# Kernel tuning notes

Hardware: AMD Instinct MI355X
Metric: run time of the kernel (lower is better)

## Reference

```python
import jax, jax.numpy as jnp
import numpy as np

VOCAB = 128
HIDDEN = 256


def setup_inputs() -> dict:
    key = jax.random.key(0)
    ks = jax.random.split(key, 8)
    B, S = 64, 2048
    # first feature channel: event-type ids stored as floats (module does .long())
    ev = jax.random.randint(ks[0], (B, S, 1), 0, VOCAB).astype(jnp.float32)
    num = jax.random.normal(ks[1], (B, S, 7), dtype=jnp.float32)
    X = jnp.concatenate([ev, num], axis=-1)  # [B,S,8]
    emb_table = jax.random.normal(ks[2], (VOCAB, 124), dtype=jnp.float32) * 0.1
    W_num = jax.random.normal(ks[3], (4, 7), dtype=jnp.float32) * 0.3
    b_num = jnp.zeros((4,), dtype=jnp.float32)
    W_conv = jax.random.normal(ks[4], (3 * HIDDEN, 128), dtype=jnp.float32) * 0.08
    b_conv = jnp.zeros((3 * HIDDEN,), dtype=jnp.float32)
    W_out = jax.random.normal(ks[5], (1, HIDDEN), dtype=jnp.float32) * 0.06
    b_out = jnp.zeros((1,), dtype=jnp.float32)
    return {"X": X, "emb_table": emb_table, "W_num": W_num, "b_num": b_num,
            "W_conv": W_conv, "b_conv": b_conv, "W_out": W_out, "b_out": b_out}


def reference(X, emb_table, W_num, b_num, W_conv, b_conv, W_out, b_out):
    # X: [B,S,8] -- channel 0 = event id, channels 1: = numeric attrs
    event = jax.lax.stop_gradient(X[:, :, 0]).astype(jnp.int32)   # [B,S]
    numeric = X[:, :, 1:]                                          # [B,S,7]
    emb = emb_table[event]                                         # [B,S,124]
    tn = numeric @ W_num.T + b_num                                 # [B,S,4]
    comb = jnp.concatenate([emb, tn], axis=-1)                     # [B,S,128]
    # Conv1d with kernel_size=1 == pointwise linear to 3*hidden gates
    gates = comb @ W_conv.T + b_conv                               # [B,S,3H]
    gates = jnp.transpose(gates, (1, 0, 2))                        # [S,B,3H]
    Z, F, O = jnp.split(gates, 3, axis=2)
    Z = jnp.tanh(Z)
    F = jax.nn.sigmoid(F)
    O = jax.nn.sigmoid(O)

    def step(h, zfo):
        z, f, o = zfo
        h = f * h + (1.0 - f) * z
        return h, o * h

    h0 = jnp.zeros(Z.shape[1:], dtype=Z.dtype)                     # [B,H]
    _, hs = jax.lax.scan(step, h0, (Z, F, O))                      # hs: [S,B,H]
    final_rep = hs[-1]                                             # [B,H]
    # dropout is identity at inference (dropout=0 / eval)
    return final_rep @ W_out.T + b_out                             # [B,1]
```

## Files before the change

### kernel.cpp

```cpp
#include <hip/hip_runtime.h>


typedef float    f32x2 __attribute__((ext_vector_type(2)));
typedef float    f32x4 __attribute__((ext_vector_type(4)));
typedef _Float16 f16x2 __attribute__((ext_vector_type(2)));

#define NB 64
#define NS 2048
#define NH 256
#define CHUNKS 32
#define STEPS (NS / CHUNKS)
#define LOG2E 1.4426950408889634f
#define PAD 129
#define JH 128

__global__ __launch_bounds__(256) void precompute_kernel(
    const float* __restrict__ X,
    const float* __restrict__ emb,
    const float* __restrict__ Wn,
    const float* __restrict__ bn,
    const float* __restrict__ Wc,
    const float* __restrict__ bc,
    f16x2* __restrict__ G2h,
    float* __restrict__ Go,
    f32x2* __restrict__ Wg4,
    float* __restrict__ Wgo4,
    f32x4* __restrict__ XpA,
    float* __restrict__ XpB)
{
    const int tid = threadIdx.x;
    const int blk = blockIdx.x;

    if (blk < 256) {
        __shared__ float M[124 * PAD];
        __shared__ float P[3][2][128];
        {
            const int e = tid >> 1, half = tid & 1;
            const f32x4* er4 = (const f32x4*)(emb + (size_t)e * 124);
            #pragma unroll
            for (int i = 0; i < 16; ++i) {
                const int idx = half * 16 + i;
                if (idx < 31) {
                    const f32x4 v = er4[idx];
                    const int k0 = idx * 4;
                    M[(k0 + 0) * PAD + e] = v.x;
                    M[(k0 + 1) * PAD + e] = v.y;
                    M[(k0 + 2) * PAD + e] = v.z;
                    M[(k0 + 3) * PAD + e] = v.w;
                }
            }
        }
        __syncthreads();

        const int e = tid & 127;
        const int h = tid >> 7;
        const int j = blk;
        const int k0 = h * 62;

        const float* __restrict__ wzr = Wc + (size_t)j * 128;
        const float* __restrict__ wfr = Wc + (size_t)(j + 256) * 128;
        const float* __restrict__ wor = Wc + (size_t)(j + 512) * 128;

        float az = 0.f, af = 0.f, ao = 0.f;
        #pragma unroll 31
        for (int i = 0; i < 62; ++i) {
            const int k = k0 + i;
            const float mv = M[k * PAD + e];
            az = fmaf(wzr[k], mv, az);
            af = fmaf(wfr[k], mv, af);
            ao = fmaf(wor[k], mv, ao);
        }
        P[0][h][e] = az; P[1][h][e] = af; P[2][h][e] = ao;
        __syncthreads();

        if (h == 0) {
            float sz = P[0][0][e] + P[0][1][e] + bc[j];
            float sf = P[1][0][e] + P[1][1][e] + bc[j + 256];
            float so = P[2][0][e] + P[2][1][e] + bc[j + 512];
            #pragma unroll
            for (int m = 0; m < 4; ++m) {
                const float bm = bn[m];
                sz = fmaf(wzr[124 + m], bm, sz);
                sf = fmaf(wfr[124 + m], bm, sf);
                so = fmaf(wor[124 + m], bm, so);
            }
            G2h[(size_t)e * NH + j] = (f16x2){(_Float16)(sz * (-2.0f * LOG2E)),
                                              (_Float16)(sf * (-LOG2E))};
            Go[(size_t)e * NH + j] = so * (-LOG2E);
        }
    } else if (blk == 256) {
        const int j = tid;
        #pragma unroll
        for (int m = 0; m < 4; ++m) {
            const float wz = Wc[(size_t)j * 128 + 124 + m];
            const float wf = Wc[(size_t)(j + 256) * 128 + 124 + m];
            const float wo = Wc[(size_t)(j + 512) * 128 + 124 + m];
            Wg4[m * NH + j]  = (f32x2){wz * (-2.0f * LOG2E), wf * (-LOG2E)};
            Wgo4[m * NH + j] = wo * (-LOG2E);
        }
    } else {
        const f32x4* X4 = (const f32x4*)X;
        float wn[4][7];
        #pragma unroll
        for (int m = 0; m < 4; ++m)
            #pragma unroll
            for (int n = 0; n < 7; ++n) wn[m][n] = Wn[m * 7 + n];

        const int base = (blk - 257) * 1024 + tid;
        #pragma unroll
        for (int u = 0; u < 4; ++u) {
            const int idx = base + u * 256;
            const f32x4 xa = X4[(size_t)idx * 2];
            const f32x4 xb = X4[(size_t)idx * 2 + 1];
            const int eo = ((int)xa.x) << 9;
            const float xs[7] = {xa.y, xa.z, xa.w, xb.x, xb.y, xb.z, xb.w};
            float y[4];
            #pragma unroll
            for (int m = 0; m < 4; ++m) {
                float s = 0.0f;
                #pragma unroll
                for (int n = 0; n < 7; ++n) s = fmaf(wn[m][n], xs[n], s);
                y[m] = s;
            }
            XpA[idx] = (f32x4){__int_as_float(eo), y[0], y[1], y[2]};
            XpB[idx] = y[3];
        }
    }
}

__global__ __launch_bounds__(1024) void scan_kernel(
    const f32x4* __restrict__ XpA,
    const float* __restrict__ XpB,
    const f16x2* __restrict__ G2h,
    const float* __restrict__ Go,
    const f32x2* __restrict__ Wg4,
    const float* __restrict__ Wgo4,
    float* __restrict__ AB,
    float* __restrict__ Olast)
{
    __shared__ f16x2 T[128 * JH];

    const int tid = threadIdx.x;
    const int jbase = blockIdx.y * JH;

    {
        const uint4* __restrict__ src = (const uint4*)G2h;
        uint4* dst = (uint4*)T;
        const int colbase = jbase >> 2;
        #pragma unroll
        for (int i = tid; i < 4096; i += 1024) {
            const int e = i >> 5, c16 = i & 31;
            dst[i] = src[e * 64 + colbase + c16];
        }
    }
    __syncthreads();

    const int slice = tid >> 7;
    const int jj = tid & (JH - 1);
    const int widx = (int)blockIdx.x * 8 + slice;
    const int b = widx >> 5;
    const int c = widx & (CHUNKS - 1);
    const int j = jbase + jj;

    const f32x4* __restrict__ xa = XpA + ((size_t)b * NS + (size_t)c * STEPS);
    const float* __restrict__ xb = XpB + ((size_t)b * NS + (size_t)c * STEPS);
    const char*  __restrict__ Tb = (const char*)T;
    const int jj4 = jj * 4;

    const f32x2 w0 = Wg4[0 * NH + j];
    const f32x2 w1 = Wg4[1 * NH + j];
    const f32x2 w2 = Wg4[2 * NH + j];
    const f32x2 w3 = Wg4[3 * NH + j];

    float A = 1.0f, Bv = 0.0f;
    #pragma unroll
    for (int t = 0; t < STEPS; ++t) {
        const f32x4 ra = xa[t];
        const float y3 = xb[t];
        const unsigned eo = (unsigned)__float_as_int(ra.x);
        const f16x2 gh = *(const f16x2*)(Tb + eo + jj4);
        f32x2 g = (f32x2){(float)gh.x, (float)gh.y};
        g = __builtin_elementwise_fma(w0, (f32x2){ra.y, ra.y}, g);
        g = __builtin_elementwise_fma(w1, (f32x2){ra.z, ra.z}, g);
        g = __builtin_elementwise_fma(w2, (f32x2){ra.w, ra.w}, g);
        g = __builtin_elementwise_fma(w3, (f32x2){y3, y3}, g);

        const float ez = __builtin_amdgcn_exp2f(g.x);
        const float ef = __builtin_amdgcn_exp2f(g.y);
        const float az = 1.0f + ez, af = 1.0f + ef;
        const float r = __builtin_amdgcn_rcpf(az * af);
        const float f = r * az;
        const float z = fmaf(2.0f, r * af, -1.0f);

        A *= f;
        Bv = fmaf(f, Bv - z, z);
    }

    AB[(((size_t)c * NB + b) * 2 + 0) * NH + j] = A;
    AB[(((size_t)c * NB + b) * 2 + 1) * NH + j] = Bv;

    if (c == CHUNKS - 1) {
        const f32x4 la = xa[STEPS - 1];
        const float ly3 = xb[STEPS - 1];
        const size_t eo = (size_t)(unsigned)__float_as_int(la.x);
        float go = *(const float*)((const char*)Go + (eo << 1) + (size_t)j * 4);
        go = fmaf(Wgo4[0 * NH + j], la.y, go);
        go = fmaf(Wgo4[1 * NH + j], la.z, go);
        go = fmaf(Wgo4[2 * NH + j], la.w, go);
        go = fmaf(Wgo4[3 * NH + j], ly3, go);
        Olast[b * NH + j] = __builtin_amdgcn_rcpf(1.0f + __builtin_amdgcn_exp2f(go));
    }
}

__global__ __launch_bounds__(256) void combine_kernel(
    const float* __restrict__ AB,
    const float* __restrict__ Olast,
    const float* __restrict__ Wout,
    const float* __restrict__ bout,
    float* __restrict__ out)
{
    const int b = blockIdx.x;
    const int j = threadIdx.x;

    float h = 0.0f;
    #pragma unroll 8
    for (int c = 0; c < CHUNKS; ++c) {
        const float A  = AB[(((size_t)c * NB + b) * 2 + 0) * NH + j];
        const float Bv = AB[(((size_t)c * NB + b) * 2 + 1) * NH + j];
        h = fmaf(A, h, Bv);
    }
    float v = Olast[b * NH + j] * h * Wout[j];

    #pragma unroll
    for (int off = 32; off > 0; off >>= 1) v += __shfl_down(v, off);
    __shared__ float red[4];
    if ((j & 63) == 0) red[j >> 6] = v;
    __syncthreads();
    if (j == 0) out[b] = red[0] + red[1] + red[2] + red[3] + bout[0];
}

extern "C" void kernel_launch(void* const* d_in, const int* in_sizes, int n_in,
                              void* d_out, int out_size, void* d_ws, size_t ws_size,
                              hipStream_t stream) {
    const float* X    = (const float*)d_in[0];
    const float* emb  = (const float*)d_in[1];
    const float* Wn   = (const float*)d_in[2];
    const float* bn   = (const float*)d_in[3];
    const float* Wc   = (const float*)d_in[4];
    const float* bc   = (const float*)d_in[5];
    const float* Wout = (const float*)d_in[6];
    const float* bout = (const float*)d_in[7];
    float* out = (float*)d_out;

    char* w = (char*)d_ws;
    f16x2* G2h  = (f16x2*)w;   w += 128 * NH * sizeof(f16x2);
    float* Go   = (float*)w;   w += 128 * NH * sizeof(float);
    f32x2* Wg4  = (f32x2*)w;   w += 4 * NH * sizeof(f32x2);
    float* Wgo4 = (float*)w;   w += 4 * NH * sizeof(float);
    float* AB   = (float*)w;   w += (size_t)CHUNKS * NB * 2 * NH * sizeof(float);
    float* Ol   = (float*)w;   w += NB * NH * sizeof(float);
    f32x4* XpA  = (f32x4*)w;   w += (size_t)NB * NS * sizeof(f32x4);
    float* XpB  = (float*)w;   w += (size_t)NB * NS * sizeof(float);

    precompute_kernel<<<385, 256, 0, stream>>>(X, emb, Wn, bn, Wc, bc,
                                               G2h, Go, Wg4, Wgo4, XpA, XpB);
    dim3 gridS(256, 2);
    scan_kernel<<<gridS, 1024, 0, stream>>>(XpA, XpB, G2h, Go, Wg4, Wgo4, AB, Ol);
    combine_kernel<<<NB, 256, 0, stream>>>(AB, Ol, Wout, bout, out);
}
```

Measured before the change: 40.39 us.

## Split scan into 64 chunks with two independent chains per thread

The scan is re-partitioned: the sequence is cut into twice as many chunks, each block covers a quarter of the hidden units, and each thread advances two independent chunk recurrences at once. The per-block LDS table slice shrinks to match the smaller hidden slice, and the event-offset encoding is adjusted to the new row stride. The aim is to shorten serial dependency chains and overlap latency through instruction-level parallelism and higher occupancy. In exchange, the combine step has more chunk partials to merge, and each thread holds more registers.

```diff
diff --git a/kernel.cpp b/kernel.cpp
--- a/kernel.cpp
+++ b/kernel.cpp
@@ -8,11 +8,11 @@
 #define NB 64
 #define NS 2048
 #define NH 256
-#define CHUNKS 32
+#define CHUNKS 64
 #define STEPS (NS / CHUNKS)
 #define LOG2E 1.4426950408889634f
 #define PAD 129
-#define JH 128
+#define JH 64
 
 __global__ __launch_bounds__(256) void precompute_kernel(
     const float* __restrict__ X,
@@ -112,7 +112,7 @@
             const int idx = base + u * 256;
             const f32x4 xa = X4[(size_t)idx * 2];
             const f32x4 xb = X4[(size_t)idx * 2 + 1];
-            const int eo = ((int)xa.x) << 9;
+            const int eo = ((int)xa.x) << 8;
             const float xs[7] = {xa.y, xa.z, xa.w, xb.x, xb.y, xb.z, xb.w};
             float y[4];
             #pragma unroll
@@ -128,7 +128,7 @@
     }
 }
 
-__global__ __launch_bounds__(1024) void scan_kernel(
+__global__ __launch_bounds__(512, 4) void scan_kernel(
     const f32x4* __restrict__ XpA,
     const float* __restrict__ XpB,
     const f16x2* __restrict__ G2h,
@@ -141,29 +141,34 @@
     __shared__ f16x2 T[128 * JH];
 
     const int tid = threadIdx.x;
-    const int jbase = blockIdx.y * JH;
+    const int jq = blockIdx.y;
+    const int jbase = jq * JH;
 
     {
         const uint4* __restrict__ src = (const uint4*)G2h;
         uint4* dst = (uint4*)T;
-        const int colbase = jbase >> 2;
-        #pragma unroll
-        for (int i = tid; i < 4096; i += 1024) {
-            const int e = i >> 5, c16 = i & 31;
+        const int colbase = jq * 16;
+        #pragma unroll
+        for (int i = tid; i < 2048; i += 512) {
+            const int e = i >> 4, c16 = i & 15;
             dst[i] = src[e * 64 + colbase + c16];
         }
     }
     __syncthreads();
 
-    const int slice = tid >> 7;
     const int jj = tid & (JH - 1);
-    const int widx = (int)blockIdx.x * 8 + slice;
-    const int b = widx >> 5;
-    const int c = widx & (CHUNKS - 1);
+    const int row = tid >> 6;
     const int j = jbase + jj;
-
-    const f32x4* __restrict__ xa = XpA + ((size_t)b * NS + (size_t)c * STEPS);
-    const float* __restrict__ xb = XpB + ((size_t)b * NS + (size_t)c * STEPS);
+    const int widx0 = (int)blockIdx.x * 16 + row;
+    const int widx1 = widx0 + 8;
+    const int b  = widx0 >> 6;
+    const int c0 = widx0 & (CHUNKS - 1);
+    const int c1 = widx1 & (CHUNKS - 1);
+
+    const f32x4* __restrict__ xa0 = XpA + ((size_t)b * NS + (size_t)c0 * STEPS);
+    const float* __restrict__ xb0 = XpB + ((size_t)b * NS + (size_t)c0 * STEPS);
+    const f32x4* __restrict__ xa1 = XpA + ((size_t)b * NS + (size_t)c1 * STEPS);
+    const float* __restrict__ xb1 = XpB + ((size_t)b * NS + (size_t)c1 * STEPS);
     const char*  __restrict__ Tb = (const char*)T;
     const int jj4 = jj * 4;
 
@@ -172,38 +177,57 @@
     const f32x2 w2 = Wg4[2 * NH + j];
     const f32x2 w3 = Wg4[3 * NH + j];
 
-    float A = 1.0f, Bv = 0.0f;
+    float A0 = 1.0f, B0 = 0.0f, A1 = 1.0f, B1 = 0.0f;
     #pragma unroll
     for (int t = 0; t < STEPS; ++t) {
-        const f32x4 ra = xa[t];
-        const float y3 = xb[t];
-        const unsigned eo = (unsigned)__float_as_int(ra.x);
-        const f16x2 gh = *(const f16x2*)(Tb + eo + jj4);
-        f32x2 g = (f32x2){(float)gh.x, (float)gh.y};
-        g = __builtin_elementwise_fma(w0, (f32x2){ra.y, ra.y}, g);
-        g = __builtin_elementwise_fma(w1, (f32x2){ra.z, ra.z}, g);
-        g = __builtin_elementwise_fma(w2, (f32x2){ra.w, ra.w}, g);
-        g = __builtin_elementwise_fma(w3, (f32x2){y3, y3}, g);
-
-        const float ez = __builtin_amdgcn_exp2f(g.x);
-        const float ef = __builtin_amdgcn_exp2f(g.y);
-        const float az = 1.0f + ez, af = 1.0f + ef;
-        const float r = __builtin_amdgcn_rcpf(az * af);
-        const float f = r * az;
-        const float z = fmaf(2.0f, r * af, -1.0f);
-
-        A *= f;
-        Bv = fmaf(f, Bv - z, z);
-    }
-
-    AB[(((size_t)c * NB + b) * 2 + 0) * NH + j] = A;
-    AB[(((size_t)c * NB + b) * 2 + 1) * NH + j] = Bv;
-
-    if (c == CHUNKS - 1) {
-        const f32x4 la = xa[STEPS - 1];
-        const float ly3 = xb[STEPS - 1];
+        const f32x4 ra0 = xa0[t];
+        const float ry0 = xb0[t];
+        const f32x4 ra1 = xa1[t];
+        const float ry1 = xb1[t];
+        const unsigned eo0 = (unsigned)__float_as_int(ra0.x);
+        const unsigned eo1 = (unsigned)__float_as_int(ra1.x);
+        const f16x2 gh0 = *(const f16x2*)(Tb + eo0 + jj4);
+        const f16x2 gh1 = *(const f16x2*)(Tb + eo1 + jj4);
+
+        f32x2 g0 = (f32x2){(float)gh0.x, (float)gh0.y};
+        g0 = __builtin_elementwise_fma(w0, (f32x2){ra0.y, ra0.y}, g0);
+        g0 = __builtin_elementwise_fma(w1, (f32x2){ra0.z, ra0.z}, g0);
+        g0 = __builtin_elementwise_fma(w2, (f32x2){ra0.w, ra0.w}, g0);
+        g0 = __builtin_elementwise_fma(w3, (f32x2){ry0, ry0}, g0);
+
+        f32x2 g1 = (f32x2){(float)gh1.x, (float)gh1.y};
+        g1 = __builtin_elementwise_fma(w0, (f32x2){ra1.y, ra1.y}, g1);
+        g1 = __builtin_elementwise_fma(w1, (f32x2){ra1.z, ra1.z}, g1);
+        g1 = __builtin_elementwise_fma(w2, (f32x2){ra1.w, ra1.w}, g1);
+        g1 = __builtin_elementwise_fma(w3, (f32x2){ry1, ry1}, g1);
+
+        const float ez0 = __builtin_amdgcn_exp2f(g0.x);
+        const float ef0 = __builtin_amdgcn_exp2f(g0.y);
+        const float ez1 = __builtin_amdgcn_exp2f(g1.x);
+        const float ef1 = __builtin_amdgcn_exp2f(g1.y);
+        const float az0 = 1.0f + ez0, af0 = 1.0f + ef0;
+        const float az1 = 1.0f + ez1, af1 = 1.0f + ef1;
+        const float r0 = __builtin_amdgcn_rcpf(az0 * af0);
+        const float r1 = __builtin_amdgcn_rcpf(az1 * af1);
+        const float f0 = r0 * az0;
+        const float f1 = r1 * az1;
+        const float z0 = fmaf(2.0f, r0 * af0, -1.0f);
+        const float z1 = fmaf(2.0f, r1 * af1, -1.0f);
+
+        A0 *= f0; B0 = fmaf(f0, B0 - z0, z0);
+        A1 *= f1; B1 = fmaf(f1, B1 - z1, z1);
+    }
+
+    AB[(((size_t)c0 * NB + b) * 2 + 0) * NH + j] = A0;
+    AB[(((size_t)c0 * NB + b) * 2 + 1) * NH + j] = B0;
+    AB[(((size_t)c1 * NB + b) * 2 + 0) * NH + j] = A1;
+    AB[(((size_t)c1 * NB + b) * 2 + 1) * NH + j] = B1;
+
+    if (c1 == CHUNKS - 1) {
+        const f32x4 la = xa1[STEPS - 1];
+        const float ly3 = xb1[STEPS - 1];
         const size_t eo = (size_t)(unsigned)__float_as_int(la.x);
-        float go = *(const float*)((const char*)Go + (eo << 1) + (size_t)j * 4);
+        float go = *(const float*)((const char*)Go + (eo << 2) + (size_t)j * 4);
         go = fmaf(Wgo4[0 * NH + j], la.y, go);
         go = fmaf(Wgo4[1 * NH + j], la.z, go);
         go = fmaf(Wgo4[2 * NH + j], la.w, go);
@@ -264,7 +288,7 @@
 
     precompute_kernel<<<385, 256, 0, stream>>>(X, emb, Wn, bn, Wc, bc,
                                                G2h, Go, Wg4, Wgo4, XpA, XpB);
-    dim3 gridS(256, 2);
-    scan_kernel<<<gridS, 1024, 0, stream>>>(XpA, XpB, G2h, Go, Wg4, Wgo4, AB, Ol);
+    dim3 gridS(256, 4);
+    scan_kernel<<<gridS, 512, 0, stream>>>(XpA, XpB, G2h, Go, Wg4, Wgo4, AB, Ol);
     combine_kernel<<<NB, 256, 0, stream>>>(AB, Ol, Wout, bout, out);
 }
```

Measured after the change: 45.29 us. 1.12x slower.

## Pack per-step inputs into one 16-byte record and software-pipeline scan loads

Applied to the files above, without the earlier changes.

The two per-step input streams (an f32x4 plus a separate float) are merged into a single 16-byte record by storing the last two numeric projections as packed fp16. The scan loop now prefetches records three steps ahead and the LDS gate lookup one step ahead, using register ring buffers with unroll 4. This aims to cut global load instructions and hide load latency in the sequential recurrence. The cost is reduced precision on two projected inputs, and reads that run past each chunk's end, which the padded buffer absorbs.

```diff
diff --git a/kernel.cpp b/kernel.cpp
--- a/kernel.cpp
+++ b/kernel.cpp
@@ -13,6 +13,8 @@
 #define LOG2E 1.4426950408889634f
 #define PAD 129
 #define JH 128
+
+union f16x2_f32 { f16x2 h; float f; };
 
 __global__ __launch_bounds__(256) void precompute_kernel(
     const float* __restrict__ X,
@@ -25,8 +27,7 @@
     float* __restrict__ Go,
     f32x2* __restrict__ Wg4,
     float* __restrict__ Wgo4,
-    f32x4* __restrict__ XpA,
-    float* __restrict__ XpB)
+    f32x4* __restrict__ Xp)
 {
     const int tid = threadIdx.x;
     const int blk = blockIdx.x;
@@ -122,15 +123,15 @@
                 for (int n = 0; n < 7; ++n) s = fmaf(wn[m][n], xs[n], s);
                 y[m] = s;
             }
-            XpA[idx] = (f32x4){__int_as_float(eo), y[0], y[1], y[2]};
-            XpB[idx] = y[3];
+            union f16x2_f32 u23;
+            u23.h = (f16x2){(_Float16)y[2], (_Float16)y[3]};
+            Xp[idx] = (f32x4){__int_as_float(eo), y[0], y[1], u23.f};
         }
     }
 }
 
 __global__ __launch_bounds__(1024) void scan_kernel(
-    const f32x4* __restrict__ XpA,
-    const float* __restrict__ XpB,
+    const f32x4* __restrict__ Xp,
     const f16x2* __restrict__ G2h,
     const float* __restrict__ Go,
     const f32x2* __restrict__ Wg4,
@@ -162,8 +163,7 @@
     const int c = widx & (CHUNKS - 1);
     const int j = jbase + jj;
 
-    const f32x4* __restrict__ xa = XpA + ((size_t)b * NS + (size_t)c * STEPS);
-    const float* __restrict__ xb = XpB + ((size_t)b * NS + (size_t)c * STEPS);
+    const f32x4* __restrict__ xa = Xp + ((size_t)b * NS + (size_t)c * STEPS);
     const char*  __restrict__ Tb = (const char*)T;
     const int jj4 = jj * 4;
 
@@ -172,17 +172,34 @@
     const f32x2 w2 = Wg4[2 * NH + j];
     const f32x2 w3 = Wg4[3 * NH + j];
 
+    f32x4 rec[4];
+    f16x2 tv[2];
+    rec[0] = xa[0];
+    rec[1] = xa[1];
+    rec[2] = xa[2];
+    {
+        const unsigned eo0 = (unsigned)__float_as_int(rec[0].x) & 0xFE00u;
+        tv[0] = *(const f16x2*)(Tb + eo0 + jj4);
+    }
+
     float A = 1.0f, Bv = 0.0f;
-    #pragma unroll
+    #pragma unroll 4
     for (int t = 0; t < STEPS; ++t) {
-        const f32x4 ra = xa[t];
-        const float y3 = xb[t];
-        const unsigned eo = (unsigned)__float_as_int(ra.x);
-        const f16x2 gh = *(const f16x2*)(Tb + eo + jj4);
+        rec[(t + 3) & 3] = xa[t + 3];
+        const unsigned eon =
+            (unsigned)__float_as_int(rec[(t + 1) & 3].x) & 0xFE00u;
+        tv[(t + 1) & 1] = *(const f16x2*)(Tb + eon + jj4);
+
+        const f32x4 ra = rec[t & 3];
+        const f16x2 gh = tv[t & 1];
+        union f16x2_f32 u23; u23.f = ra.w;
+        const float y2 = (float)u23.h.x;
+        const float y3 = (float)u23.h.y;
+
         f32x2 g = (f32x2){(float)gh.x, (float)gh.y};
         g = __builtin_elementwise_fma(w0, (f32x2){ra.y, ra.y}, g);
         g = __builtin_elementwise_fma(w1, (f32x2){ra.z, ra.z}, g);
-        g = __builtin_elementwise_fma(w2, (f32x2){ra.w, ra.w}, g);
+        g = __builtin_elementwise_fma(w2, (f32x2){y2, y2}, g);
         g = __builtin_elementwise_fma(w3, (f32x2){y3, y3}, g);
 
         const float ez = __builtin_amdgcn_exp2f(g.x);
@@ -201,13 +218,13 @@
 
     if (c == CHUNKS - 1) {
         const f32x4 la = xa[STEPS - 1];
-        const float ly3 = xb[STEPS - 1];
-        const size_t eo = (size_t)(unsigned)__float_as_int(la.x);
+        union f16x2_f32 u23; u23.f = la.w;
+        const size_t eo = (size_t)((unsigned)__float_as_int(la.x) & 0xFE00u);
         float go = *(const float*)((const char*)Go + (eo << 1) + (size_t)j * 4);
         go = fmaf(Wgo4[0 * NH + j], la.y, go);
         go = fmaf(Wgo4[1 * NH + j], la.z, go);
-        go = fmaf(Wgo4[2 * NH + j], la.w, go);
-        go = fmaf(Wgo4[3 * NH + j], ly3, go);
+        go = fmaf(Wgo4[2 * NH + j], (float)u23.h.x, go);
+        go = fmaf(Wgo4[3 * NH + j], (float)u23.h.y, go);
         Olast[b * NH + j] = __builtin_amdgcn_rcpf(1.0f + __builtin_amdgcn_exp2f(go));
     }
 }
@@ -259,12 +276,11 @@
     float* Wgo4 = (float*)w;   w += 4 * NH * sizeof(float);
     float* AB   = (float*)w;   w += (size_t)CHUNKS * NB * 2 * NH * sizeof(float);
     float* Ol   = (float*)w;   w += NB * NH * sizeof(float);
-    f32x4* XpA  = (f32x4*)w;   w += (size_t)NB * NS * sizeof(f32x4);
-    float* XpB  = (float*)w;   w += (size_t)NB * NS * sizeof(float);
+    f32x4* Xp   = (f32x4*)w;   w += ((size_t)NB * NS + 4) * sizeof(f32x4);
 
     precompute_kernel<<<385, 256, 0, stream>>>(X, emb, Wn, bn, Wc, bc,
-                                               G2h, Go, Wg4, Wgo4, XpA, XpB);
+                                               G2h, Go, Wg4, Wgo4, Xp);
     dim3 gridS(256, 2);
-    scan_kernel<<<gridS, 1024, 0, stream>>>(XpA, XpB, G2h, Go, Wg4, Wgo4, AB, Ol);
+    scan_kernel<<<gridS, 1024, 0, stream>>>(Xp, G2h, Go, Wg4, Wgo4, AB, Ol);
     combine_kernel<<<NB, 256, 0, stream>>>(AB, Ol, Wout, bout, out);
 }
```

New measurement: 41.97 us. 3.9% more time.
